# Optimization experiments

Hardware: AMD Instinct MI355X
Metric: run time of the kernel (lower is better)

The kernel has to match this reference:

```python
import jax, jax.numpy as jnp
import numpy as np

C = 32          # backbone_channels[-4]
RATIO = 0.05    # keep_topk ratio

def conv2d(x, w, b, pad, groups=1):
    y = jax.lax.conv_general_dilated(x, w, (1, 1), [(pad, pad), (pad, pad)],
                                     dimension_numbers=('NCHW', 'OIHW', 'NCHW'),
                                     feature_group_count=groups)
    return y + b[None, :, None, None]

def bn(x, g, b, m, v, eps=1e-5):
    return (x - m[None, :, None, None]) * jax.lax.rsqrt(v[None, :, None, None] + eps) \
           * g[None, :, None, None] + b[None, :, None, None]

def up2x_bilinear(x):
    B, Ch, H, W = x.shape
    return jax.image.resize(x, (B, Ch, 2 * H, 2 * W), method='bilinear')

def setup_inputs() -> dict:
    key = jax.random.key(0)
    ks = jax.random.split(key, 20)
    f32 = jnp.float32
    d = {
        'feats4x': jax.random.normal(ks[0], (16, C, 128, 128), f32),
        'feats2x': jax.random.normal(ks[1], (16, 16, 256, 256), f32),
        'classify_logits': jax.random.normal(ks[2], (16, 1, 256, 256), f32),
        # SparseConvNeXtBlock params
        'dw_w': jax.random.normal(ks[3], (C, 1, 7, 7), f32) * 0.05,
        'dw_b': jnp.zeros((C,), f32),
        'ln_g': jnp.ones((C,), f32), 'ln_b': jnp.zeros((C,), f32),
        'pw1_w': jax.random.normal(ks[4], (C, C), f32) * 0.05, 'pw1_b': jnp.zeros((C,), f32),
        'grn_g': jnp.ones((C,), f32) * 0.1, 'grn_b': jnp.zeros((C,), f32),
        'pw2_w': jax.random.normal(ks[5], (C, C), f32) * 0.05, 'pw2_b': jnp.zeros((C,), f32),
        'up_w': jax.random.normal(ks[6], (8, C, 3, 3), f32) * 0.05, 'up_b': jnp.zeros((8,), f32),
        'bn1_g': jnp.ones((8,), f32), 'bn1_b': jnp.zeros((8,), f32),
        'bn1_m': jnp.zeros((8,), f32), 'bn1_v': jnp.ones((8,), f32),
        'sh_w': jax.random.normal(ks[7], (8, 16, 3, 3), f32) * 0.05, 'sh_b': jnp.zeros((8,), f32),
        'bn2_g': jnp.ones((8,), f32), 'bn2_b': jnp.zeros((8,), f32),
        'bn2_m': jnp.zeros((8,), f32), 'bn2_v': jnp.ones((8,), f32),
        'last_w': jax.random.normal(ks[8], (4, 16, 3, 3), f32) * 0.05, 'last_b': jnp.zeros((4,), f32),
        'last2_w': jax.random.normal(ks[9], (1, 4, 5, 5), f32) * 0.05, 'last2_b': jnp.zeros((1,), f32),
    }
    return d

def _forward(feats4x, feats2x, classify_logits,
             dw_w, dw_b, ln_g, ln_b, pw1_w, pw1_b, grn_g, grn_b, pw2_w, pw2_b,
             up_w, up_b, bn1_g, bn1_b, bn1_m, bn1_v,
             sh_w, sh_b, bn2_g, bn2_b, bn2_m, bn2_v,
             last_w, last_b, last2_w, last2_b):
    prob = jax.nn.sigmoid(classify_logits[:, :, ::2, ::2])  # [B,1,H4,W4]
    B, _, H, W = prob.shape
    k = int(RATIO * H * W)
    flat = prob.reshape(B, -1)
    vals, _ = jax.lax.top_k(flat, k)
    thr = vals[:, -1]
    mask = (flat > thr[:, None]).reshape(B, 1, H, W).astype(feats4x.dtype)

    # --- SparseConvNeXtBlock (mlp_ratio=1, linear_pw_conv, GRN, layer_scale=0) ---
    shortcut = feats4x
    x = conv2d(feats4x, dw_w, dw_b, 3, groups=C) * mask     # sparse dwconv 7x7
    xh = x.transpose(0, 2, 3, 1)                            # NHWC
    mu = xh.mean(-1, keepdims=True)
    var = ((xh - mu) ** 2).mean(-1, keepdims=True)
    xh = (xh - mu) * jax.lax.rsqrt(var + 1e-6) * ln_g + ln_b
    xh = xh * mask.transpose(0, 2, 3, 1)                    # sparse LN2d
    xh = xh @ pw1_w.T + pw1_b
    xh = jax.nn.gelu(xh, approximate=False)
    gx = jnp.sqrt(jnp.sum(xh ** 2, axis=(1, 2), keepdims=True))  # GRN, [B,1,1,C]
    nx = gx / (jnp.mean(gx, axis=-1, keepdims=True) + 1e-6)
    xh = grn_g * (xh * nx) + grn_b + xh
    xh = xh @ pw2_w.T + pw2_b
    x = shortcut + xh.transpose(0, 3, 1, 2)

    # --- upsample module (part of sparse_head list) ---
    x = up2x_bilinear(bn(conv2d(x, up_w, up_b, 1), bn1_g, bn1_b, bn1_m, bn1_v))  # [B,8,H2,W2]
    s = jax.nn.relu(bn(conv2d(feats2x, sh_w, sh_b, 1), bn2_g, bn2_b, bn2_m, bn2_v))
    out = jnp.concatenate([x, s], axis=1)                   # [B,16,H2,W2]
    out = up2x_bilinear(conv2d(out, last_w, last_b, 1))     # [B,4,H,W]
    out = conv2d(out, last2_w, last2_b, 2)                  # [B,1,H,W]
    return jax.nn.sigmoid(out), jax.nn.sigmoid(classify_logits)

def reference(feats4x, feats2x, classify_logits,
              dw_w, dw_b, ln_g, ln_b, pw1_w, pw1_b, grn_g, grn_b, pw2_w, pw2_b,
              up_w, up_b, bn1_g, bn1_b, bn1_m, bn1_v,
              sh_w, sh_b, bn2_g, bn2_b, bn2_m, bn2_v,
              last_w, last_b, last2_w, last2_b):
    return _forward(feats4x, feats2x, classify_logits,
                    dw_w, dw_b, ln_g, ln_b, pw1_w, pw1_b, grn_g, grn_b, pw2_w, pw2_b,
                    up_w, up_b, bn1_g, bn1_b, bn1_m, bn1_v,
                    sh_w, sh_b, bn2_g, bn2_b, bn2_m, bn2_v,
                    last_w, last_b, last2_w, last2_b)
```

## Files before the change

### kernel.cpp

```cpp
#include <hip/hip_runtime.h>
#include <math.h>


#define NSLOT 824

typedef __attribute__((ext_vector_type(4))) float f32x4;

struct __attribute__((packed, aligned(4))) f4u { float a0, a1, a2, a3; };

__device__ __forceinline__ void nt_store4(float* p, float a, float b, float c,
                                          float d) {
  f32x4 v = {a, b, c, d};
  __builtin_nontemporal_store(v, reinterpret_cast<f32x4*>(p));
}

__device__ __forceinline__ float erf_fast(float x) {
  float ax = fabsf(x);
  float t = __builtin_amdgcn_rcpf(fmaf(0.3275911f, ax, 1.f));
  float poly = t * fmaf(t, fmaf(t, fmaf(t, fmaf(t, 1.061405429f, -1.453152027f),
                                        1.421413741f), -0.284496736f), 0.254829592f);
  float r = 1.f - poly * __expf(-ax * ax);
  return copysignf(r, x);
}

__global__ void k_sig(const float* __restrict__ lg, float* __restrict__ out) {
  int i = blockIdx.x * 256 + threadIdx.x;
  float4 v = reinterpret_cast<const float4*>(lg)[i];
  nt_store4(out + (i << 2), 1.f / (1.f + __expf(-v.x)), 1.f / (1.f + __expf(-v.y)),
            1.f / (1.f + __expf(-v.z)), 1.f / (1.f + __expf(-v.w)));
}

__global__ __launch_bounds__(1024) void k_topk(const float* __restrict__ lg,
                                               int* __restrict__ actIdx,
                                               int* __restrict__ n_act) {
  __shared__ unsigned keys[16384];
  __shared__ unsigned hist[256];
  __shared__ unsigned sh_prefix, sh_krem;
  __shared__ int sh_cnt;
  int b = blockIdx.x, t = threadIdx.x;
  if (t < 256) hist[t] = 0u;
  if (t == 0) { sh_prefix = 0u; sh_krem = 819u; sh_cnt = 0; }
  __syncthreads();
  for (int i = t; i < 16384; i += 1024) {
    float vF = lg[(b << 16) + ((i >> 7) << 9) + ((i & 127) << 1)];
    unsigned u = __float_as_uint(vF);
    unsigned key = (u & 0x80000000u) ? ~u : (u | 0x80000000u);
    keys[i] = key;
    atomicAdd(&hist[key >> 24], 1u);
  }
  for (int pass = 0; pass < 4; ++pass) {
    __syncthreads();
    if (t == 0) {
      unsigned krem = sh_krem, c = 0;
      int bin = 255;
      for (; bin >= 0; --bin) {
        unsigned c2 = c + hist[bin];
        if (c2 >= krem) break;
        c = c2;
      }
      sh_prefix = (sh_prefix << 8) | (unsigned)bin;
      sh_krem = krem - c;
    }
    __syncthreads();
    if (pass < 3) {
      if (t < 256) hist[t] = 0u;
      __syncthreads();
      int shift = 16 - 8 * pass;
      unsigned pref = sh_prefix;
      for (int i = t; i < 16384; i += 1024) {
        unsigned key = keys[i];
        if ((key >> (shift + 8)) == pref) atomicAdd(&hist[(key >> shift) & 255u], 1u);
      }
    }
  }
  __syncthreads();
  unsigned thrkey = sh_prefix;
  for (int i = t; i < 16384; i += 1024) {
    if (keys[i] > thrkey) {
      int s = atomicAdd(&sh_cnt, 1);
      actIdx[b * NSLOT + s] = i;
    }
  }
  __syncthreads();
  if (t == 0) n_act[b] = sh_cnt;
}

__global__ __launch_bounds__(256, 4) void k_dws(
    const float* __restrict__ f4, const int* __restrict__ actIdx,
    const int* __restrict__ n_act, const float* __restrict__ dw_w,
    const float* __restrict__ dw_b, const float* __restrict__ lng,
    const float* __restrict__ lnb, const float* __restrict__ w1,
    const float* __restrict__ b1, float* __restrict__ y1c,
    float* __restrict__ gss) {
  int b = blockIdx.y;
  int slot0 = blockIdx.x << 3;
  int na = n_act[b];
  if (slot0 >= na) return;
  int t = threadIdx.x;
  __shared__ float wdwT[49][32];
  __shared__ float w1sT[32][32];
  __shared__ float xhs[8][32];
  __shared__ float pacc[8][32];
  __shared__ float sLng[32], sLnb[32], sB1[32], sDwB[32];
  for (int i = t; i < 1568; i += 256) wdwT[i % 49][i / 49] = dw_w[i];
  for (int i = t; i < 1024; i += 256) w1sT[i & 31][i >> 5] = w1[i];
  if (t < 32) { sLng[t] = lng[t]; sLnb[t] = lnb[t]; sB1[t] = b1[t]; sDwB[t] = dw_b[t]; }
  __syncthreads();
  int px = t >> 5, c = t & 31;
  int slot = slot0 + px;
  bool valid = slot < na;
  int pos = valid ? actIdx[b * NSLOT + slot] : -1;
  float xv = 0.f;
  if (valid) {
    int y = pos >> 7, x = pos & 127;
    const float* base = f4 + (((b << 5) + c) << 14);
    float a = sDwB[c];
    bool inner = (x >= 3) && (x <= 123);
#pragma unroll
    for (int dy = -3; dy <= 3; ++dy) {
      int yy = y + dy;
      if ((unsigned)yy < 128u) {
        const float* rp = base + (yy << 7) + x;
        if (inner) {
          f4u A4 = *reinterpret_cast<const f4u*>(rp - 3);
          f4u B4 = *reinterpret_cast<const f4u*>(rp + 1);
          float r[7] = {A4.a0, A4.a1, A4.a2, A4.a3, B4.a0, B4.a1, B4.a2};
#pragma unroll
          for (int k = 0; k < 7; ++k)
            a = fmaf(r[k], wdwT[(dy + 3) * 7 + k][c], a);
        } else {
#pragma unroll
          for (int k = 0; k < 7; ++k) {
            int xx = x - 3 + k;
            if ((unsigned)xx < 128u)
              a = fmaf(rp[k - 3], wdwT[(dy + 3) * 7 + k][c], a);
          }
        }
      }
    }
    xv = a;
  }
  float s1 = xv, s2 = xv * xv;
#pragma unroll
  for (int m = 1; m < 32; m <<= 1) {
    s1 += __shfl_xor(s1, m, 64);
    s2 += __shfl_xor(s2, m, 64);
  }
  float mu = s1 * 0.03125f;
  float var = fmaxf(s2 * 0.03125f - mu * mu, 0.f);
  float rs = rsqrtf(var + 1e-6f);
  float xh = (xv - mu) * rs * sLng[c] + sLnb[c];
  xhs[px][c] = valid ? xh : 0.f;
  __syncthreads();
  int j = c;
  float a = sB1[j];
#pragma unroll
  for (int cc = 0; cc < 32; ++cc) a = fmaf(xhs[px][cc], w1sT[cc][j], a);
  float gl = 0.5f * a * (1.f + erf_fast(a * 0.70710678f));
  pacc[px][j] = valid ? gl * gl : 0.f;
  if (valid) y1c[(b * NSLOT + slot) * 32 + j] = gl;
  __syncthreads();
  if (t < 32) {
    float s = 0.f;
#pragma unroll
    for (int q = 0; q < 8; ++q) s += pacc[q][t];
    atomicAdd(&gss[(b << 5) + t], s);
  }
}

__global__ void k_grn(const float* __restrict__ gss, const int* __restrict__ n_act,
                      const float* __restrict__ grng, const float* __restrict__ grnb,
                      const float* __restrict__ w2, const float* __restrict__ b2,
                      const float* __restrict__ b1, float* __restrict__ w2sT,
                      float* __restrict__ bias2, float* __restrict__ Kconst) {
  int b = blockIdx.x, t = threadIdx.x;
  __shared__ float gxs[32], sc[32], gb1[32];
  if (t < 32) {
    float u = b1[t];
    float gl = 0.5f * u * (1.f + erf_fast(u * 0.70710678f));
    gb1[t] = gl;
    float cnt = (float)(16384 - n_act[b]);
    gxs[t] = sqrtf(gss[(b << 5) + t] + cnt * gl * gl);
  }
  __syncthreads();
  if (t < 32) {
    float m = 0.f;
#pragma unroll
    for (int c = 0; c < 32; ++c) m += gxs[c];
    m = m * 0.03125f + 1e-6f;
    sc[t] = grng[t] * (gxs[t] / m) + 1.f;
  }
  __syncthreads();
  for (int i = t; i < 1024; i += 256) {
    int c = i >> 5, j = i & 31;
    w2sT[(b << 10) + i] = w2[j * 32 + c] * sc[c];
  }
  if (t < 32) {
    float s = 0.f;
#pragma unroll
    for (int c = 0; c < 32; ++c) s += grnb[c] * w2[t * 32 + c];
    float bb = s + b2[t];
    bias2[(b << 5) + t] = bb;
    float k = bb;
#pragma unroll
    for (int c = 0; c < 32; ++c) k = fmaf(gb1[c] * sc[c], w2[t * 32 + c], k);
    Kconst[(b << 5) + t] = k;
  }
}

__global__ __launch_bounds__(256, 4) void k_pw2s(
    const float* __restrict__ y1c, const int* __restrict__ actIdx,
    const int* __restrict__ n_act, const float* __restrict__ w2sT,
    const float* __restrict__ bias2, const float* __restrict__ f4,
    float* __restrict__ xact) {
  int b = blockIdx.y;
  int slot0 = blockIdx.x << 3;
  int na = n_act[b];
  if (slot0 >= na) return;
  int t = threadIdx.x;
  __shared__ float w2s[32][32];
  __shared__ float ys[8][32];
  __shared__ float sb2[32];
  for (int i = t; i < 1024; i += 256) w2s[i >> 5][i & 31] = w2sT[(b << 10) + i];
  if (t < 32) sb2[t] = bias2[(b << 5) + t];
  int px = t >> 5, j = t & 31;
  int slot = slot0 + px;
  bool valid = slot < na;
  ys[px][j] = valid ? y1c[(b * NSLOT + slot) * 32 + j] : 0.f;
  __syncthreads();
  if (valid) {
    int pos = actIdx[b * NSLOT + slot];
    float a = sb2[j];
#pragma unroll
    for (int cc = 0; cc < 32; ++cc) a = fmaf(ys[px][cc], w2s[cc][j], a);
    a += f4[(((b << 5) + j) << 14) + pos];
    xact[(b * NSLOT + slot) * 32 + j] = a;
  }
}

__global__ __launch_bounds__(256, 4) void k_upconv(
    const float* __restrict__ f4, const float* __restrict__ Kc,
    const float* __restrict__ xact, const int* __restrict__ actIdx,
    const int* __restrict__ n_act, const float* __restrict__ wgt,
    const float* __restrict__ bias, const float* __restrict__ bng,
    const float* __restrict__ bnb, const float* __restrict__ bnm,
    const float* __restrict__ bnv, float* __restrict__ out) {
  int bx = blockIdx.x << 4, by = blockIdx.y << 4, b = blockIdx.z;
  int t = threadIdx.x;
  __shared__ __align__(16) float4 xt[18 * 19];
  __shared__ __align__(16) float4 wt[576];
  __shared__ unsigned short slotmap[324];
  __shared__ float sKc[32];
  for (int idx = t; idx < 576; idx += 256) {
    int g = idx / 72, rem = idx - g * 72;
    int tap = rem >> 3, o = rem & 7;
    int ky = tap / 3, kx = tap - ky * 3;
    float4 wv;
    wv.x = wgt[((o * 32 + g * 4 + 0) * 3 + ky) * 3 + kx];
    wv.y = wgt[((o * 32 + g * 4 + 1) * 3 + ky) * 3 + kx];
    wv.z = wgt[((o * 32 + g * 4 + 2) * 3 + ky) * 3 + kx];
    wv.w = wgt[((o * 32 + g * 4 + 3) * 3 + ky) * 3 + kx];
    wt[idx] = wv;
  }
  if (t < 32) sKc[t] = Kc[(b << 5) + t];
  for (int i = t; i < 324; i += 256) slotmap[i] = 0xFFFFu;
  __syncthreads();
  int na = n_act[b];
  for (int i = t; i < na; i += 256) {
    int pos = actIdx[b * NSLOT + i];
    int y = pos >> 7, x = pos & 127;
    unsigned r = (unsigned)(y - by + 1), c = (unsigned)(x - bx + 1);
    if (r < 18u && c < 18u) slotmap[r * 18 + c] = (unsigned short)i;
  }
  __syncthreads();
  int py = t >> 4, px = t & 15;
  float acc[8];
#pragma unroll
  for (int o = 0; o < 8; ++o) acc[o] = 0.f;
  float4 sr[2];
  auto loadg = [&](int g) {
#pragma unroll
    for (int k = 0; k < 2; ++k) {
      int i = t + (k << 8);
      float4 v = make_float4(0.f, 0.f, 0.f, 0.f);
      if (i < 324) {
        int r = i / 18, c = i - r * 18;
        int gy = by - 1 + r, gx = bx - 1 + c;
        if ((unsigned)gy < 128u && (unsigned)gx < 128u) {
          unsigned short s = slotmap[r * 18 + c];
          if (s != 0xFFFFu) {
            v = *reinterpret_cast<const float4*>(
                xact + ((b * NSLOT + (int)s) << 5) + (g << 2));
          } else {
            const float* p0 = f4 + (((b << 5) + (g << 2)) << 14) + (gy << 7) + gx;
            v.x = p0[0] + sKc[(g << 2) + 0];
            v.y = p0[16384] + sKc[(g << 2) + 1];
            v.z = p0[32768] + sKc[(g << 2) + 2];
            v.w = p0[49152] + sKc[(g << 2) + 3];
          }
        }
      }
      sr[k] = v;
    }
  };
  auto writeg = [&]() {
#pragma unroll
    for (int k = 0; k < 2; ++k) {
      int i = t + (k << 8);
      if (i < 324) {
        int r = i / 18;
        xt[r * 19 + (i - r * 18)] = sr[k];
      }
    }
  };
  loadg(0);
#pragma unroll 1
  for (int g = 0; g < 8; ++g) {
    writeg();
    __syncthreads();
    if (g < 7) loadg(g + 1);
#pragma unroll
    for (int ky = 0; ky < 3; ++ky) {
      float4 xr[3];
#pragma unroll
      for (int q = 0; q < 3; ++q) xr[q] = xt[(py + ky) * 19 + px + q];
#pragma unroll
      for (int kx = 0; kx < 3; ++kx)
#pragma unroll
        for (int o = 0; o < 8; ++o) {
          float4 wv = wt[(g * 9 + ky * 3 + kx) * 8 + o];
          float4 xv = xr[kx];
          acc[o] = fmaf(xv.w, wv.w, fmaf(xv.z, wv.z, fmaf(xv.y, wv.y, fmaf(xv.x, wv.x, acc[o]))));
        }
    }
    __syncthreads();
  }
  int gy = by + py, gx = bx + px;
  float ov[8];
#pragma unroll
  for (int o = 0; o < 8; ++o) {
    float rs = rsqrtf(bnv[o] + 1e-5f) * bng[o];
    ov[o] = acc[o] * rs + (bias[o] - bnm[o]) * rs + bnb[o];
  }
  float* op = out + (((b << 14) + (gy << 7) + gx) << 3);
  *reinterpret_cast<float4*>(op) = make_float4(ov[0], ov[1], ov[2], ov[3]);
  *reinterpret_cast<float4*>(op + 4) = make_float4(ov[4], ov[5], ov[6], ov[7]);
}

__global__ __launch_bounds__(256, 4) void k_conv3s(
    const float* __restrict__ xin,
    const float* __restrict__ wgt, const float* __restrict__ bias,
    const float* __restrict__ bng, const float* __restrict__ bnb,
    const float* __restrict__ bnm, const float* __restrict__ bnv,
    float* __restrict__ out) {
  int bx = blockIdx.x << 5, by = blockIdx.y << 5, b = blockIdx.z;
  int t = threadIdx.x;
  int py = t >> 3, px0 = (t & 7) << 2;
  __shared__ __align__(16) float4 xt[34 * 35];
  __shared__ __align__(16) float4 wt[4 * 9 * 8];
  for (int idx = t; idx < 288; idx += 256) {
    int g = idx / 72, rem = idx - g * 72;
    int tap = rem >> 3, o = rem & 7;
    int ky = tap / 3, kx = tap - ky * 3;
    float4 wv;
    wv.x = wgt[((o * 16 + g * 4 + 0) * 3 + ky) * 3 + kx];
    wv.y = wgt[((o * 16 + g * 4 + 1) * 3 + ky) * 3 + kx];
    wv.z = wgt[((o * 16 + g * 4 + 2) * 3 + ky) * 3 + kx];
    wv.w = wgt[((o * 16 + g * 4 + 3) * 3 + ky) * 3 + kx];
    wt[idx] = wv;
  }
  float acc[4][8];
#pragma unroll
  for (int i = 0; i < 4; ++i)
#pragma unroll
    for (int o = 0; o < 8; ++o) acc[i][o] = 0.f;

  float4 sr[5];
  auto loadg = [&](int g) {
#pragma unroll
    for (int k = 0; k < 5; ++k) {
      int i = t + (k << 8);
      float4 v = make_float4(0.f, 0.f, 0.f, 0.f);
      if (i < 1156) {
        int r = i / 34, c = i - r * 34;
        int gy = by - 1 + r, gx = bx - 1 + c;
        if ((unsigned)gy < 256u && (unsigned)gx < 256u) {
          const float* p0 = xin + (((b * 16 + (g << 2)) << 8) + gy) * 256 + gx;
          v.x = p0[0]; v.y = p0[65536]; v.z = p0[131072]; v.w = p0[196608];
        }
      }
      sr[k] = v;
    }
  };
  auto writeg = [&]() {
#pragma unroll
    for (int k = 0; k < 5; ++k) {
      int i = t + (k << 8);
      if (i < 1156) {
        int r = i / 34;
        xt[r * 35 + (i - r * 34)] = sr[k];
      }
    }
  };

  loadg(0);
#pragma unroll 1
  for (int g = 0; g < 4; ++g) {
    writeg();
    __syncthreads();
    if (g < 3) loadg(g + 1);
#pragma unroll
    for (int ky = 0; ky < 3; ++ky) {
      float4 xr[6];
#pragma unroll
      for (int q = 0; q < 6; ++q) xr[q] = xt[(py + ky) * 35 + px0 + q];
#pragma unroll
      for (int kx = 0; kx < 3; ++kx)
#pragma unroll
        for (int o = 0; o < 8; ++o) {
          float4 wv = wt[(g * 9 + ky * 3 + kx) * 8 + o];
#pragma unroll
          for (int i = 0; i < 4; ++i) {
            float4 xv = xr[kx + i];
            acc[i][o] = fmaf(xv.w, wv.w, fmaf(xv.z, wv.z, fmaf(xv.y, wv.y, fmaf(xv.x, wv.x, acc[i][o]))));
          }
        }
    }
    __syncthreads();
  }
  float scl[8], sbs[8];
#pragma unroll
  for (int o = 0; o < 8; ++o) {
    float rs = rsqrtf(bnv[o] + 1e-5f) * bng[o];
    scl[o] = rs;
    sbs[o] = (bias[o] - bnm[o]) * rs + bnb[o];
  }
  int gy = by + py;
#pragma unroll
  for (int i = 0; i < 4; ++i) {
    int gx = bx + px0 + i;
    float ov[8];
#pragma unroll
    for (int o = 0; o < 8; ++o)
      ov[o] = fmaxf(acc[i][o] * scl[o] + sbs[o], 0.f);
    float* op = out + (((b << 16) + (gy << 8) + gx) << 3);
    *reinterpret_cast<float4*>(op) = make_float4(ov[0], ov[1], ov[2], ov[3]);
    *reinterpret_cast<float4*>(op + 4) = make_float4(ov[4], ov[5], ov[6], ov[7]);
  }
}

__global__ __launch_bounds__(256, 3) void k_lastup(
    const float* __restrict__ E, const float* __restrict__ D,
    const float* __restrict__ wgt, const float* __restrict__ bias,
    float* __restrict__ out) {
  int bx = blockIdx.x << 5, by = blockIdx.y << 5, b = blockIdx.z;
  int t = threadIdx.x;
  int py = t >> 3, px0 = (t & 7) << 2;
  __shared__ __align__(16) float4 et[19][22][2];
  __shared__ __align__(16) float4 xt[34 * 35];
  __shared__ __align__(16) float4 wt[144];
  for (int idx = t; idx < 144; idx += 256) {
    int g = idx / 36, rem = idx - g * 36;
    int tap = rem >> 2, o = rem & 3;
    int ky = tap / 3, kx = tap - ky * 3;
    float4 wv;
    wv.x = wgt[((o * 16 + g * 4 + 0) * 3 + ky) * 3 + kx];
    wv.y = wgt[((o * 16 + g * 4 + 1) * 3 + ky) * 3 + kx];
    wv.z = wgt[((o * 16 + g * 4 + 2) * 3 + ky) * 3 + kx];
    wv.w = wgt[((o * 16 + g * 4 + 3) * 3 + ky) * 3 + kx];
    wt[idx] = wv;
  }
  float acc[4][4];
#pragma unroll
  for (int i = 0; i < 4; ++i)
#pragma unroll
    for (int o = 0; o < 4; ++o) acc[i][o] = 0.f;

  float4 dreg[5];
  auto loadD = [&](int h) {
#pragma unroll
    for (int k = 0; k < 5; ++k) {
      int i = t + (k << 8);
      float4 v = make_float4(0.f, 0.f, 0.f, 0.f);
      if (i < 1156) {
        int r = i / 34, c = i - r * 34;
        int gy = by - 1 + r, gx = bx - 1 + c;
        if ((unsigned)gy < 256u && (unsigned)gx < 256u)
          v = *reinterpret_cast<const float4*>(
              D + (((b << 16) + (gy << 8) + gx) << 3) + (h << 2));
      }
      dreg[k] = v;
    }
  };
  auto compute = [&](int g) {
#pragma unroll
    for (int ky = 0; ky < 3; ++ky) {
      float4 xr[6];
#pragma unroll
      for (int q = 0; q < 6; ++q) xr[q] = xt[(py + ky) * 35 + px0 + q];
#pragma unroll
      for (int kx = 0; kx < 3; ++kx)
#pragma unroll
        for (int o = 0; o < 4; ++o) {
          float4 wv = wt[(g * 9 + ky * 3 + kx) * 4 + o];
#pragma unroll
          for (int i = 0; i < 4; ++i) {
            float4 xv = xr[kx + i];
            acc[i][o] = fmaf(xv.w, wv.w, fmaf(xv.z, wv.z, fmaf(xv.y, wv.y, fmaf(xv.x, wv.x, acc[i][o]))));
          }
        }
    }
  };

  loadD(0);
  int ey0 = (by >> 1) - 1, ex0 = (bx >> 1) - 3;
#pragma unroll
  for (int k = 0; k < 4; ++k) {
    int i = t + (k << 8);
    if (i < 836) {
      int h = i & 1, q = i >> 1;
      int r = q / 22, c = q - r * 22;
      int er = min(max(ey0 + r, 0), 127), ec = min(max(ex0 + c, 0), 127);
      et[r][c][h] = *reinterpret_cast<const float4*>(
          E + (((b << 14) + (er << 7) + ec) << 3) + (h << 2));
    }
  }
#pragma unroll 1
  for (int h = 0; h < 2; ++h) {
    __syncthreads();
#pragma unroll
    for (int k = 0; k < 5; ++k) {
      int i = t + (k << 8);
      if (i < 1156) {
        int r = i / 34;
        xt[r * 35 + (i - r * 34)] = dreg[k];
      }
    }
    __syncthreads();
    if (h == 0) loadD(1);
    compute(2 + h);
  }
#pragma unroll 1
  for (int h = 0; h < 2; ++h) {
    __syncthreads();
#pragma unroll
    for (int k = 0; k < 5; ++k) {
      int i = t + (k << 8);
      if (i < 1156) {
        int r = i / 34, c = i - r * 34;
        int gy = by - 1 + r, gx = bx - 1 + c;
        float4 uv = make_float4(0.f, 0.f, 0.f, 0.f);
        if ((unsigned)gy < 256u && (unsigned)gx < 256u) {
          int r0 = (gy - 1) >> 1, c0 = (gx - 1) >> 1;
          float fy = (gy & 1) ? 0.25f : 0.75f;
          float fx = (gx & 1) ? 0.25f : 0.75f;
          int ra = max(r0, 0) - ey0, rb = min(r0 + 1, 127) - ey0;
          int ca = max(c0, 0) - ex0, cb = min(c0 + 1, 127) - ex0;
          float w00 = (1.f - fy) * (1.f - fx), w01 = (1.f - fy) * fx;
          float w10 = fy * (1.f - fx), w11 = fy * fx;
          float4 a = et[ra][ca][h], bq = et[ra][cb][h];
          float4 cq = et[rb][ca][h], dq = et[rb][cb][h];
          uv.x = w00 * a.x + w01 * bq.x + w10 * cq.x + w11 * dq.x;
          uv.y = w00 * a.y + w01 * bq.y + w10 * cq.y + w11 * dq.y;
          uv.z = w00 * a.z + w01 * bq.z + w10 * cq.z + w11 * dq.z;
          uv.w = w00 * a.w + w01 * bq.w + w10 * cq.w + w11 * dq.w;
        }
        xt[r * 35 + c] = uv;
      }
    }
    __syncthreads();
    compute(h);
  }
  float b0 = bias[0], b1v = bias[1], b2v = bias[2], b3v = bias[3];
  int gy = by + py;
#pragma unroll
  for (int i = 0; i < 4; ++i) {
    int gx = bx + px0 + i;
    float* op = out + (((b << 16) + (gy << 8) + gx) << 2);
    *reinterpret_cast<float4*>(op) = make_float4(acc[i][0] + b0, acc[i][1] + b1v,
                                                 acc[i][2] + b2v, acc[i][3] + b3v);
  }
}

__global__ __launch_bounds__(256, 3) void k_final(
    const float* __restrict__ v4, const float* __restrict__ w5,
    const float* __restrict__ b5, float* __restrict__ out) {
  int bx = blockIdx.x << 5, by = blockIdx.y << 5, b = blockIdx.z;
  int t = threadIdx.x;
  __shared__ __align__(16) float4 vt[20 * 21];
  __shared__ __align__(16) float4 ut[36 * 37];
  __shared__ __align__(16) float4 w5s[25];
  if (t < 25) {
    w5s[t] = make_float4(w5[t], w5[25 + t], w5[50 + t], w5[75 + t]);
  }
  int vy0 = (by >> 1) - 2, vx0 = (bx >> 1) - 2;
  for (int i = t; i < 400; i += 256) {
    int r = i / 20, c = i - r * 20;
    int gy = vy0 + r, gx = vx0 + c;
    float4 v = make_float4(0.f, 0.f, 0.f, 0.f);
    if (gy >= 0 && gy < 256 && gx >= 0 && gx < 256)
      v = *reinterpret_cast<const float4*>(v4 + ((b << 16) + gy * 256 + gx) * 4);
    vt[r * 21 + c] = v;
  }
  __syncthreads();
  for (int i = t; i < 36 * 36; i += 256) {
    int r = i / 36, c = i - r * 36;
    int yy = by - 2 + r, xx = bx - 2 + c;
    float4 uv = make_float4(0.f, 0.f, 0.f, 0.f);
    if (yy >= 0 && yy < 512 && xx >= 0 && xx < 512) {
      int r0 = (yy - 1) >> 1, c0 = (xx - 1) >> 1;
      float fy = (yy & 1) ? 0.25f : 0.75f;
      float fx = (xx & 1) ? 0.25f : 0.75f;
      int ra = max(r0, 0) - vy0, rb = min(r0 + 1, 255) - vy0;
      int ca = max(c0, 0) - vx0, cb = min(c0 + 1, 255) - vx0;
      float4 a = vt[ra * 21 + ca], bq = vt[ra * 21 + cb];
      float4 cq = vt[rb * 21 + ca], dq = vt[rb * 21 + cb];
      float w00 = (1.f - fy) * (1.f - fx), w01 = (1.f - fy) * fx;
      float w10 = fy * (1.f - fx), w11 = fy * fx;
      uv.x = w00 * a.x + w01 * bq.x + w10 * cq.x + w11 * dq.x;
      uv.y = w00 * a.y + w01 * bq.y + w10 * cq.y + w11 * dq.y;
      uv.z = w00 * a.z + w01 * bq.z + w10 * cq.z + w11 * dq.z;
      uv.w = w00 * a.w + w01 * bq.w + w10 * cq.w + w11 * dq.w;
    }
    ut[r * 37 + c] = uv;
  }
  __syncthreads();
  float bb = b5[0];
  int py = t >> 3, px0 = (t & 7) << 2;
  float a0 = bb, a1 = bb, a2 = bb, a3 = bb;
#pragma unroll
  for (int ky = 0; ky < 5; ++ky) {
    float4 xr[8];
#pragma unroll
    for (int q = 0; q < 8; ++q) xr[q] = ut[(py + ky) * 37 + px0 + q];
#pragma unroll
    for (int kx = 0; kx < 5; ++kx) {
      float4 w = w5s[ky * 5 + kx];
      float4 x0 = xr[kx], x1 = xr[kx + 1], x2 = xr[kx + 2], x3 = xr[kx + 3];
      a0 = fmaf(x0.w, w.w, fmaf(x0.z, w.z, fmaf(x0.y, w.y, fmaf(x0.x, w.x, a0))));
      a1 = fmaf(x1.w, w.w, fmaf(x1.z, w.z, fmaf(x1.y, w.y, fmaf(x1.x, w.x, a1))));
      a2 = fmaf(x2.w, w.w, fmaf(x2.z, w.z, fmaf(x2.y, w.y, fmaf(x2.x, w.x, a2))));
      a3 = fmaf(x3.w, w.w, fmaf(x3.z, w.z, fmaf(x3.y, w.y, fmaf(x3.x, w.x, a3))));
    }
  }
  int oy = by + py, ox = bx + px0;
  nt_store4(out + (b << 18) + oy * 512 + ox,
            1.f / (1.f + __expf(-a0)), 1.f / (1.f + __expf(-a1)),
            1.f / (1.f + __expf(-a2)), 1.f / (1.f + __expf(-a3)));
}

extern "C" void kernel_launch(void* const* d_in, const int* in_sizes, int n_in,
                              void* d_out, int out_size, void* d_ws, size_t ws_size,
                              hipStream_t stream) {
  (void)in_sizes; (void)n_in; (void)out_size; (void)ws_size;
  const float* feats4x = (const float*)d_in[0];
  const float* feats2x = (const float*)d_in[1];
  const float* clg     = (const float*)d_in[2];
  const float* dw_w    = (const float*)d_in[3];
  const float* dw_b    = (const float*)d_in[4];
  const float* ln_g    = (const float*)d_in[5];
  const float* ln_b    = (const float*)d_in[6];
  const float* pw1_w   = (const float*)d_in[7];
  const float* pw1_b   = (const float*)d_in[8];
  const float* grn_g   = (const float*)d_in[9];
  const float* grn_b   = (const float*)d_in[10];
  const float* pw2_w   = (const float*)d_in[11];
  const float* pw2_b   = (const float*)d_in[12];
  const float* up_w    = (const float*)d_in[13];
  const float* up_b    = (const float*)d_in[14];
  const float* bn1_g   = (const float*)d_in[15];
  const float* bn1_b   = (const float*)d_in[16];
  const float* bn1_m   = (const float*)d_in[17];
  const float* bn1_v   = (const float*)d_in[18];
  const float* sh_w    = (const float*)d_in[19];
  const float* sh_b    = (const float*)d_in[20];
  const float* bn2_g   = (const float*)d_in[21];
  const float* bn2_b   = (const float*)d_in[22];
  const float* bn2_m   = (const float*)d_in[23];
  const float* bn2_v   = (const float*)d_in[24];
  const float* last_w  = (const float*)d_in[25];
  const float* last_b  = (const float*)d_in[26];
  const float* last2_w = (const float*)d_in[27];
  const float* last2_b = (const float*)d_in[28];
  float* outp = (float*)d_out;
  float* ws = (float*)d_ws;
  float* A      = ws;
  float* y1c    = ws + 8388608;
  float* xact   = ws + 8810496;
  int*   actIdx = (int*)(ws + 9232384);
  int*   n_act  = (int*)(ws + 9245568);
  float* D      = ws + 16777216;
  float* E      = ws + 25165824;
  float* gss    = ws + 27262976;
  float* w2sT   = gss + 512;
  float* bias2  = w2sT + 16384;
  float* Kconst = bias2 + 512;

  hipMemsetAsync(gss, 0, 512 * sizeof(float), stream);
  k_sig<<<1024, 256, 0, stream>>>(clg, outp + 4194304);
  k_topk<<<16, 1024, 0, stream>>>(clg, actIdx, n_act);
  k_dws<<<dim3(103, 16), 256, 0, stream>>>(feats4x, actIdx, n_act, dw_w, dw_b,
                                           ln_g, ln_b, pw1_w, pw1_b, y1c, gss);
  k_grn<<<16, 256, 0, stream>>>(gss, n_act, grn_g, grn_b, pw2_w, pw2_b, pw1_b,
                                w2sT, bias2, Kconst);
  k_pw2s<<<dim3(103, 16), 256, 0, stream>>>(y1c, actIdx, n_act, w2sT, bias2,
                                            feats4x, xact);
  k_upconv<<<dim3(8, 8, 16), 256, 0, stream>>>(feats4x, Kconst, xact, actIdx,
                                               n_act, up_w, up_b, bn1_g, bn1_b,
                                               bn1_m, bn1_v, E);
  k_conv3s<<<dim3(8, 8, 16), 256, 0, stream>>>(feats2x, sh_w, sh_b, bn2_g,
                                               bn2_b, bn2_m, bn2_v, D);
  k_lastup<<<dim3(8, 8, 16), 256, 0, stream>>>(E, D, last_w, last_b, A);
  k_final<<<dim3(16, 16, 16), 256, 0, stream>>>(A, last2_w, last2_b, outp);
}
```

Before: 259.7 us.

## Merge upconv, shortcut conv and sigmoid into one heterogeneous launch

Three independent kernels (sparse-path up conv, feats2x shortcut conv with BN/ReLU, and classify-logit sigmoid) are combined into a single launch whose blocks pick their role from blockIdx.z. This removes two kernel launches and the idle tail between them, so small grids can fill the GPU together. In exchange, shared memory per block becomes the sum of both conv tiles, which may lower occupancy for every block role, and register pressure becomes the maximum of the branches.

```diff
diff --git a/kernel.cpp b/kernel.cpp
--- a/kernel.cpp
+++ b/kernel.cpp
@@ -21,13 +21,6 @@
                                         1.421413741f), -0.284496736f), 0.254829592f);
   float r = 1.f - poly * __expf(-ax * ax);
   return copysignf(r, x);
-}
-
-__global__ void k_sig(const float* __restrict__ lg, float* __restrict__ out) {
-  int i = blockIdx.x * 256 + threadIdx.x;
-  float4 v = reinterpret_cast<const float4*>(lg)[i];
-  nt_store4(out + (i << 2), 1.f / (1.f + __expf(-v.x)), 1.f / (1.f + __expf(-v.y)),
-            1.f / (1.f + __expf(-v.z)), 1.f / (1.f + __expf(-v.w)));
 }
 
 __global__ __launch_bounds__(1024) void k_topk(const float* __restrict__ lg,
@@ -238,212 +231,225 @@
   }
 }
 
-__global__ __launch_bounds__(256, 4) void k_upconv(
+__global__ __launch_bounds__(256, 4) void k_mid(
     const float* __restrict__ f4, const float* __restrict__ Kc,
     const float* __restrict__ xact, const int* __restrict__ actIdx,
-    const int* __restrict__ n_act, const float* __restrict__ wgt,
-    const float* __restrict__ bias, const float* __restrict__ bng,
-    const float* __restrict__ bnb, const float* __restrict__ bnm,
-    const float* __restrict__ bnv, float* __restrict__ out) {
-  int bx = blockIdx.x << 4, by = blockIdx.y << 4, b = blockIdx.z;
-  int t = threadIdx.x;
-  __shared__ __align__(16) float4 xt[18 * 19];
-  __shared__ __align__(16) float4 wt[576];
+    const int* __restrict__ n_act, const float* __restrict__ up_wgt,
+    const float* __restrict__ up_bias, const float* __restrict__ bn1g,
+    const float* __restrict__ bn1b, const float* __restrict__ bn1m,
+    const float* __restrict__ bn1v, float* __restrict__ E,
+    const float* __restrict__ f2x, const float* __restrict__ sh_wgt,
+    const float* __restrict__ sh_bias, const float* __restrict__ bn2g,
+    const float* __restrict__ bn2b, const float* __restrict__ bn2m,
+    const float* __restrict__ bn2v, float* __restrict__ D,
+    const float* __restrict__ lg, float* __restrict__ out2) {
+  __shared__ __align__(16) float4 xtA[34 * 35];
+  __shared__ __align__(16) float4 wtA[288];
+  __shared__ __align__(16) float4 xtB[18 * 19];
+  __shared__ __align__(16) float4 wtB[576];
   __shared__ unsigned short slotmap[324];
   __shared__ float sKc[32];
-  for (int idx = t; idx < 576; idx += 256) {
-    int g = idx / 72, rem = idx - g * 72;
-    int tap = rem >> 3, o = rem & 7;
-    int ky = tap / 3, kx = tap - ky * 3;
-    float4 wv;
-    wv.x = wgt[((o * 32 + g * 4 + 0) * 3 + ky) * 3 + kx];
-    wv.y = wgt[((o * 32 + g * 4 + 1) * 3 + ky) * 3 + kx];
-    wv.z = wgt[((o * 32 + g * 4 + 2) * 3 + ky) * 3 + kx];
-    wv.w = wgt[((o * 32 + g * 4 + 3) * 3 + ky) * 3 + kx];
-    wt[idx] = wv;
-  }
-  if (t < 32) sKc[t] = Kc[(b << 5) + t];
-  for (int i = t; i < 324; i += 256) slotmap[i] = 0xFFFFu;
-  __syncthreads();
-  int na = n_act[b];
-  for (int i = t; i < na; i += 256) {
-    int pos = actIdx[b * NSLOT + i];
-    int y = pos >> 7, x = pos & 127;
-    unsigned r = (unsigned)(y - by + 1), c = (unsigned)(x - bx + 1);
-    if (r < 18u && c < 18u) slotmap[r * 18 + c] = (unsigned short)i;
-  }
-  __syncthreads();
-  int py = t >> 4, px = t & 15;
-  float acc[8];
-#pragma unroll
-  for (int o = 0; o < 8; ++o) acc[o] = 0.f;
-  float4 sr[2];
-  auto loadg = [&](int g) {
-#pragma unroll
-    for (int k = 0; k < 2; ++k) {
-      int i = t + (k << 8);
-      float4 v = make_float4(0.f, 0.f, 0.f, 0.f);
-      if (i < 324) {
-        int r = i / 18, c = i - r * 18;
-        int gy = by - 1 + r, gx = bx - 1 + c;
-        if ((unsigned)gy < 128u && (unsigned)gx < 128u) {
-          unsigned short s = slotmap[r * 18 + c];
-          if (s != 0xFFFFu) {
-            v = *reinterpret_cast<const float4*>(
-                xact + ((b * NSLOT + (int)s) << 5) + (g << 2));
-          } else {
-            const float* p0 = f4 + (((b << 5) + (g << 2)) << 14) + (gy << 7) + gx;
-            v.x = p0[0] + sKc[(g << 2) + 0];
-            v.y = p0[16384] + sKc[(g << 2) + 1];
-            v.z = p0[32768] + sKc[(g << 2) + 2];
-            v.w = p0[49152] + sKc[(g << 2) + 3];
+  int z = blockIdx.z;
+  int t = threadIdx.x;
+
+  if (z >= 32) {
+    int id = (((z - 32) << 6) + (blockIdx.y << 3) + blockIdx.x) * 256 + t;
+    float4 v = reinterpret_cast<const float4*>(lg)[id];
+    nt_store4(out2 + (id << 2),
+              1.f / (1.f + __expf(-v.x)), 1.f / (1.f + __expf(-v.y)),
+              1.f / (1.f + __expf(-v.z)), 1.f / (1.f + __expf(-v.w)));
+    return;
+  }
+
+  if (z >= 16) {
+    int b = z - 16;
+    int bx = blockIdx.x << 5, by = blockIdx.y << 5;
+    int py = t >> 3, px0 = (t & 7) << 2;
+    for (int idx = t; idx < 288; idx += 256) {
+      int g = idx / 72, rem = idx - g * 72;
+      int tap = rem >> 3, o = rem & 7;
+      int ky = tap / 3, kx = tap - ky * 3;
+      float4 wv;
+      wv.x = sh_wgt[((o * 16 + g * 4 + 0) * 3 + ky) * 3 + kx];
+      wv.y = sh_wgt[((o * 16 + g * 4 + 1) * 3 + ky) * 3 + kx];
+      wv.z = sh_wgt[((o * 16 + g * 4 + 2) * 3 + ky) * 3 + kx];
+      wv.w = sh_wgt[((o * 16 + g * 4 + 3) * 3 + ky) * 3 + kx];
+      wtA[idx] = wv;
+    }
+    float acc[4][8];
+#pragma unroll
+    for (int i = 0; i < 4; ++i)
+#pragma unroll
+      for (int o = 0; o < 8; ++o) acc[i][o] = 0.f;
+    float4 sr[5];
+    auto loadg = [&](int g) {
+#pragma unroll
+      for (int k = 0; k < 5; ++k) {
+        int i = t + (k << 8);
+        float4 v = make_float4(0.f, 0.f, 0.f, 0.f);
+        if (i < 1156) {
+          int r = i / 34, c = i - r * 34;
+          int gy = by - 1 + r, gx = bx - 1 + c;
+          if ((unsigned)gy < 256u && (unsigned)gx < 256u) {
+            const float* p0 = f2x + (((b * 16 + (g << 2)) << 8) + gy) * 256 + gx;
+            v.x = p0[0]; v.y = p0[65536]; v.z = p0[131072]; v.w = p0[196608];
           }
         }
-      }
-      sr[k] = v;
-    }
-  };
-  auto writeg = [&]() {
-#pragma unroll
-    for (int k = 0; k < 2; ++k) {
-      int i = t + (k << 8);
-      if (i < 324) {
-        int r = i / 18;
-        xt[r * 19 + (i - r * 18)] = sr[k];
-      }
-    }
-  };
-  loadg(0);
+        sr[k] = v;
+      }
+    };
+    auto writeg = [&]() {
+#pragma unroll
+      for (int k = 0; k < 5; ++k) {
+        int i = t + (k << 8);
+        if (i < 1156) {
+          int r = i / 34;
+          xtA[r * 35 + (i - r * 34)] = sr[k];
+        }
+      }
+    };
+    loadg(0);
 #pragma unroll 1
-  for (int g = 0; g < 8; ++g) {
-    writeg();
+    for (int g = 0; g < 4; ++g) {
+      writeg();
+      __syncthreads();
+      if (g < 3) loadg(g + 1);
+#pragma unroll
+      for (int ky = 0; ky < 3; ++ky) {
+        float4 xr[6];
+#pragma unroll
+        for (int q = 0; q < 6; ++q) xr[q] = xtA[(py + ky) * 35 + px0 + q];
+#pragma unroll
+        for (int kx = 0; kx < 3; ++kx)
+#pragma unroll
+          for (int o = 0; o < 8; ++o) {
+            float4 wv = wtA[(g * 9 + ky * 3 + kx) * 8 + o];
+#pragma unroll
+            for (int i = 0; i < 4; ++i) {
+              float4 xv = xr[kx + i];
+              acc[i][o] = fmaf(xv.w, wv.w, fmaf(xv.z, wv.z, fmaf(xv.y, wv.y, fmaf(xv.x, wv.x, acc[i][o]))));
+            }
+          }
+      }
+      __syncthreads();
+    }
+    float scl[8], sbs[8];
+#pragma unroll
+    for (int o = 0; o < 8; ++o) {
+      float rs = rsqrtf(bn2v[o] + 1e-5f) * bn2g[o];
+      scl[o] = rs;
+      sbs[o] = (sh_bias[o] - bn2m[o]) * rs + bn2b[o];
+    }
+    int gy = by + py;
+#pragma unroll
+    for (int i = 0; i < 4; ++i) {
+      int gx = bx + px0 + i;
+      float ov[8];
+#pragma unroll
+      for (int o = 0; o < 8; ++o)
+        ov[o] = fmaxf(acc[i][o] * scl[o] + sbs[o], 0.f);
+      float* op = D + (((b << 16) + (gy << 8) + gx) << 3);
+      *reinterpret_cast<float4*>(op) = make_float4(ov[0], ov[1], ov[2], ov[3]);
+      *reinterpret_cast<float4*>(op + 4) = make_float4(ov[4], ov[5], ov[6], ov[7]);
+    }
+    return;
+  }
+
+  {
+    int b = z;
+    int bx = blockIdx.x << 4, by = blockIdx.y << 4;
+    for (int idx = t; idx < 576; idx += 256) {
+      int g = idx / 72, rem = idx - g * 72;
+      int tap = rem >> 3, o = rem & 7;
+      int ky = tap / 3, kx = tap - ky * 3;
+      float4 wv;
+      wv.x = up_wgt[((o * 32 + g * 4 + 0) * 3 + ky) * 3 + kx];
+      wv.y = up_wgt[((o * 32 + g * 4 + 1) * 3 + ky) * 3 + kx];
+      wv.z = up_wgt[((o * 32 + g * 4 + 2) * 3 + ky) * 3 + kx];
+      wv.w = up_wgt[((o * 32 + g * 4 + 3) * 3 + ky) * 3 + kx];
+      wtB[idx] = wv;
+    }
+    if (t < 32) sKc[t] = Kc[(b << 5) + t];
+    for (int i = t; i < 324; i += 256) slotmap[i] = 0xFFFFu;
     __syncthreads();
-    if (g < 7) loadg(g + 1);
-#pragma unroll
-    for (int ky = 0; ky < 3; ++ky) {
-      float4 xr[3];
-#pragma unroll
-      for (int q = 0; q < 3; ++q) xr[q] = xt[(py + ky) * 19 + px + q];
-#pragma unroll
-      for (int kx = 0; kx < 3; ++kx)
-#pragma unroll
-        for (int o = 0; o < 8; ++o) {
-          float4 wv = wt[(g * 9 + ky * 3 + kx) * 8 + o];
-          float4 xv = xr[kx];
-          acc[o] = fmaf(xv.w, wv.w, fmaf(xv.z, wv.z, fmaf(xv.y, wv.y, fmaf(xv.x, wv.x, acc[o]))));
-        }
+    int na = n_act[b];
+    for (int i = t; i < na; i += 256) {
+      int pos = actIdx[b * NSLOT + i];
+      int y = pos >> 7, x = pos & 127;
+      unsigned r = (unsigned)(y - by + 1), c = (unsigned)(x - bx + 1);
+      if (r < 18u && c < 18u) slotmap[r * 18 + c] = (unsigned short)i;
     }
     __syncthreads();
-  }
-  int gy = by + py, gx = bx + px;
-  float ov[8];
-#pragma unroll
-  for (int o = 0; o < 8; ++o) {
-    float rs = rsqrtf(bnv[o] + 1e-5f) * bng[o];
-    ov[o] = acc[o] * rs + (bias[o] - bnm[o]) * rs + bnb[o];
-  }
-  float* op = out + (((b << 14) + (gy << 7) + gx) << 3);
-  *reinterpret_cast<float4*>(op) = make_float4(ov[0], ov[1], ov[2], ov[3]);
-  *reinterpret_cast<float4*>(op + 4) = make_float4(ov[4], ov[5], ov[6], ov[7]);
-}
-
-__global__ __launch_bounds__(256, 4) void k_conv3s(
-    const float* __restrict__ xin,
-    const float* __restrict__ wgt, const float* __restrict__ bias,
-    const float* __restrict__ bng, const float* __restrict__ bnb,
-    const float* __restrict__ bnm, const float* __restrict__ bnv,
-    float* __restrict__ out) {
-  int bx = blockIdx.x << 5, by = blockIdx.y << 5, b = blockIdx.z;
-  int t = threadIdx.x;
-  int py = t >> 3, px0 = (t & 7) << 2;
-  __shared__ __align__(16) float4 xt[34 * 35];
-  __shared__ __align__(16) float4 wt[4 * 9 * 8];
-  for (int idx = t; idx < 288; idx += 256) {
-    int g = idx / 72, rem = idx - g * 72;
-    int tap = rem >> 3, o = rem & 7;
-    int ky = tap / 3, kx = tap - ky * 3;
-    float4 wv;
-    wv.x = wgt[((o * 16 + g * 4 + 0) * 3 + ky) * 3 + kx];
-    wv.y = wgt[((o * 16 + g * 4 + 1) * 3 + ky) * 3 + kx];
-    wv.z = wgt[((o * 16 + g * 4 + 2) * 3 + ky) * 3 + kx];
-    wv.w = wgt[((o * 16 + g * 4 + 3) * 3 + ky) * 3 + kx];
-    wt[idx] = wv;
-  }
-  float acc[4][8];
-#pragma unroll
-  for (int i = 0; i < 4; ++i)
-#pragma unroll
-    for (int o = 0; o < 8; ++o) acc[i][o] = 0.f;
-
-  float4 sr[5];
-  auto loadg = [&](int g) {
-#pragma unroll
-    for (int k = 0; k < 5; ++k) {
-      int i = t + (k << 8);
-      float4 v = make_float4(0.f, 0.f, 0.f, 0.f);
-      if (i < 1156) {
-        int r = i / 34, c = i - r * 34;
-        int gy = by - 1 + r, gx = bx - 1 + c;
-        if ((unsigned)gy < 256u && (unsigned)gx < 256u) {
-          const float* p0 = xin + (((b * 16 + (g << 2)) << 8) + gy) * 256 + gx;
-          v.x = p0[0]; v.y = p0[65536]; v.z = p0[131072]; v.w = p0[196608];
-        }
-      }
-      sr[k] = v;
-    }
-  };
-  auto writeg = [&]() {
-#pragma unroll
-    for (int k = 0; k < 5; ++k) {
-      int i = t + (k << 8);
-      if (i < 1156) {
-        int r = i / 34;
-        xt[r * 35 + (i - r * 34)] = sr[k];
-      }
-    }
-  };
-
-  loadg(0);
-#pragma unroll 1
-  for (int g = 0; g < 4; ++g) {
-    writeg();
-    __syncthreads();
-    if (g < 3) loadg(g + 1);
-#pragma unroll
-    for (int ky = 0; ky < 3; ++ky) {
-      float4 xr[6];
-#pragma unroll
-      for (int q = 0; q < 6; ++q) xr[q] = xt[(py + ky) * 35 + px0 + q];
-#pragma unroll
-      for (int kx = 0; kx < 3; ++kx)
-#pragma unroll
-        for (int o = 0; o < 8; ++o) {
-          float4 wv = wt[(g * 9 + ky * 3 + kx) * 8 + o];
-#pragma unroll
-          for (int i = 0; i < 4; ++i) {
-            float4 xv = xr[kx + i];
-            acc[i][o] = fmaf(xv.w, wv.w, fmaf(xv.z, wv.z, fmaf(xv.y, wv.y, fmaf(xv.x, wv.x, acc[i][o]))));
+    int py = t >> 4, px = t & 15;
+    float acc[8];
+#pragma unroll
+    for (int o = 0; o < 8; ++o) acc[o] = 0.f;
+    float4 sr[2];
+    auto loadg = [&](int g) {
+#pragma unroll
+      for (int k = 0; k < 2; ++k) {
+        int i = t + (k << 8);
+        float4 v = make_float4(0.f, 0.f, 0.f, 0.f);
+        if (i < 324) {
+          int r = i / 18, c = i - r * 18;
+          int gy = by - 1 + r, gx = bx - 1 + c;
+          if ((unsigned)gy < 128u && (unsigned)gx < 128u) {
+            unsigned short s = slotmap[r * 18 + c];
+            if (s != 0xFFFFu) {
+              v = *reinterpret_cast<const float4*>(
+                  xact + ((b * NSLOT + (int)s) << 5) + (g << 2));
+            } else {
+              const float* p0 = f4 + (((b << 5) + (g << 2)) << 14) + (gy << 7) + gx;
+              v.x = p0[0] + sKc[(g << 2) + 0];
+              v.y = p0[16384] + sKc[(g << 2) + 1];
+              v.z = p0[32768] + sKc[(g << 2) + 2];
+              v.w = p0[49152] + sKc[(g << 2) + 3];
+            }
           }
         }
-    }
-    __syncthreads();
-  }
-  float scl[8], sbs[8];
-#pragma unroll
-  for (int o = 0; o < 8; ++o) {
-    float rs = rsqrtf(bnv[o] + 1e-5f) * bng[o];
-    scl[o] = rs;
-    sbs[o] = (bias[o] - bnm[o]) * rs + bnb[o];
-  }
-  int gy = by + py;
-#pragma unroll
-  for (int i = 0; i < 4; ++i) {
-    int gx = bx + px0 + i;
+        sr[k] = v;
+      }
+    };
+    auto writeg = [&]() {
+#pragma unroll
+      for (int k = 0; k < 2; ++k) {
+        int i = t + (k << 8);
+        if (i < 324) {
+          int r = i / 18;
+          xtB[r * 19 + (i - r * 18)] = sr[k];
+        }
+      }
+    };
+    loadg(0);
+#pragma unroll 1
+    for (int g = 0; g < 8; ++g) {
+      writeg();
+      __syncthreads();
+      if (g < 7) loadg(g + 1);
+#pragma unroll
+      for (int ky = 0; ky < 3; ++ky) {
+        float4 xr[3];
+#pragma unroll
+        for (int q = 0; q < 3; ++q) xr[q] = xtB[(py + ky) * 19 + px + q];
+#pragma unroll
+        for (int kx = 0; kx < 3; ++kx)
+#pragma unroll
+          for (int o = 0; o < 8; ++o) {
+            float4 wv = wtB[(g * 9 + ky * 3 + kx) * 8 + o];
+            float4 xv = xr[kx];
+            acc[o] = fmaf(xv.w, wv.w, fmaf(xv.z, wv.z, fmaf(xv.y, wv.y, fmaf(xv.x, wv.x, acc[o]))));
+          }
+      }
+      __syncthreads();
+    }
+    int gy = by + py, gx = bx + px;
     float ov[8];
 #pragma unroll
-    for (int o = 0; o < 8; ++o)
-      ov[o] = fmaxf(acc[i][o] * scl[o] + sbs[o], 0.f);
-    float* op = out + (((b << 16) + (gy << 8) + gx) << 3);
+    for (int o = 0; o < 8; ++o) {
+      float rs = rsqrtf(bn1v[o] + 1e-5f) * bn1g[o];
+      ov[o] = acc[o] * rs + (up_bias[o] - bn1m[o]) * rs + bn1b[o];
+    }
+    float* op = E + (((b << 14) + (gy << 7) + gx) << 3);
     *reinterpret_cast<float4*>(op) = make_float4(ov[0], ov[1], ov[2], ov[3]);
     *reinterpret_cast<float4*>(op + 4) = make_float4(ov[4], ov[5], ov[6], ov[7]);
   }
@@ -697,7 +703,6 @@
   float* Kconst = bias2 + 512;
 
   hipMemsetAsync(gss, 0, 512 * sizeof(float), stream);
-  k_sig<<<1024, 256, 0, stream>>>(clg, outp + 4194304);
   k_topk<<<16, 1024, 0, stream>>>(clg, actIdx, n_act);
   k_dws<<<dim3(103, 16), 256, 0, stream>>>(feats4x, actIdx, n_act, dw_w, dw_b,
                                            ln_g, ln_b, pw1_w, pw1_b, y1c, gss);
@@ -705,11 +710,10 @@
                                 w2sT, bias2, Kconst);
   k_pw2s<<<dim3(103, 16), 256, 0, stream>>>(y1c, actIdx, n_act, w2sT, bias2,
                                             feats4x, xact);
-  k_upconv<<<dim3(8, 8, 16), 256, 0, stream>>>(feats4x, Kconst, xact, actIdx,
-                                               n_act, up_w, up_b, bn1_g, bn1_b,
-                                               bn1_m, bn1_v, E);
-  k_conv3s<<<dim3(8, 8, 16), 256, 0, stream>>>(feats2x, sh_w, sh_b, bn2_g,
-                                               bn2_b, bn2_m, bn2_v, D);
+  k_mid<<<dim3(8, 8, 48), 256, 0, stream>>>(
+      feats4x, Kconst, xact, actIdx, n_act, up_w, up_b, bn1_g, bn1_b, bn1_m,
+      bn1_v, E, feats2x, sh_w, sh_b, bn2_g, bn2_b, bn2_m, bn2_v, D, clg,
+      outp + 4194304);
   k_lastup<<<dim3(8, 8, 16), 256, 0, stream>>>(E, D, last_w, last_b, A);
   k_final<<<dim3(16, 16, 16), 256, 0, stream>>>(A, last2_w, last2_b, outp);
 }
```

Result: slower. 267.4 us (+3.0%).
